# Optimization experiments

Measured on AMD Instinct MI355X. Metric: run time of the kernel, lower is better.

The kernel has to match this reference:

```python
import jax, jax.numpy as jnp
import numpy as np

TOP_K = 2
SCALING = 32.0 / 64.0  # lora_alpha / reservoir_size


def setup_inputs() -> dict:
    key = jax.random.key(0)
    ks = jax.random.split(key, 6)
    Bsz, S, Din, Dout, R, E = 4, 2048, 4096, 4096, 64, 16
    x = jax.random.normal(ks[0], (Bsz, S, Din), dtype=jnp.float32)
    base_w = jax.random.normal(ks[1], (Dout, Din), dtype=jnp.float32) * 0.02
    base_b = jax.random.normal(ks[2], (Dout,), dtype=jnp.float32) * 0.02
    A = jax.random.normal(ks[3], (R, Din), dtype=jnp.float32) * (1.0 / np.sqrt(Din))
    B = jax.random.normal(ks[4], (E, Dout, R), dtype=jnp.float32) * 0.02
    router_w = jax.random.normal(ks[5], (E, Din), dtype=jnp.float32) * 0.02
    return {"x": x, "base_w": base_w, "base_b": base_b, "A": A, "B": B, "router_w": router_w}


def reference(x, base_w, base_b, A, B, router_w):
    # base linear: [b,s,din] @ [dout,din]^T + bias
    base_out = jnp.einsum('bsi,oi->bso', x, base_w) + base_b
    # low-rank projection through fixed reservoir A (activation=identity, dropout off)
    res_hidden = jnp.einsum('bsi,ri->bsr', x, A)          # [b,s,r]
    # routing
    logits = jnp.einsum('bsi,ei->bse', x, router_w)       # [b,s,E]
    probs = jax.nn.softmax(logits, axis=-1)
    topw, topi = jax.lax.top_k(probs, TOP_K)              # [b,s,k]
    topw = topw / (jnp.sum(topw, axis=-1, keepdims=True) + 1e-6)
    num_experts = B.shape[0]
    # combine weights per expert: sum_k w_k * onehot(idx_k)  -> [b,s,E]
    combine = jnp.sum(jax.nn.one_hot(topi, num_experts, dtype=x.dtype) * topw[..., None], axis=-2)
    # weighted per-expert lowrank B matmul and combine
    delta = jnp.einsum('bse,bsr,eor->bso', combine, res_hidden, B)
    return base_out + delta * SCALING
```

## Files before the change

### kernel.cpp

```cpp
#include <hip/hip_runtime.h>
#include <cstdint>
#include <cstddef>

typedef short short8 __attribute__((ext_vector_type(8)));
typedef float f32x4 __attribute__((ext_vector_type(4)));
typedef float f32x16 __attribute__((ext_vector_type(16)));

#define DIN  4096
#define DOUT 4096
#define RANK 64
#define NEXP 16
#define NTOK 8192
#define KCAT 5120
#define NKT  (KCAT / 64)
#define ROWB (KCAT * 2)

__device__ __forceinline__ unsigned short f2bf(float f) {
    unsigned int u = __builtin_bit_cast(unsigned int, f);
    u = (u + 0x7FFFu + ((u >> 16) & 1u)) >> 16;
    return (unsigned short)u;
}
__device__ __forceinline__ void async_cp16(const void* g, void* lds) {
    __builtin_amdgcn_global_load_lds(
        (const __attribute__((address_space(1))) void*)g,
        (__attribute__((address_space(3))) void*)lds, 16, 0, 0);
}

__global__ void __launch_bounds__(256) prep_all_kernel(
        const float* __restrict__ x, const float* __restrict__ rw,
        const float* __restrict__ bw, const float* __restrict__ Bm,
        const float* __restrict__ Am,
        unsigned short* __restrict__ Xcat, unsigned short* __restrict__ Wcat,
        unsigned short* __restrict__ W1A, float* __restrict__ Lg) {
    __shared__ __align__(16) float xsl[8][532];
    __shared__ __align__(16) float red[8][16][16];
    const int tid = threadIdx.x;

    if (blockIdx.x < 1024) {
        const int t0 = blockIdx.x * 8;
        const int tt = tid >> 5, l32 = tid & 31;
        const int eg = tid >> 6, ts = (tid >> 4) & 3, cc = tid & 15;
        float part[2][4] = {};

        for (int w = 0; w < 8; ++w) {
            #pragma unroll
            for (int sub = 0; sub < 4; ++sub) {
                const int col = w * 512 + sub * 128 + l32 * 4;
                const float4 xv = *(const float4*)&x[(size_t)(t0 + tt) * DIN + col];
                unsigned short b0 = f2bf(xv.x), b1 = f2bf(xv.y),
                               b2 = f2bf(xv.z), b3 = f2bf(xv.w);
                uint2 pk = { (unsigned)b0 | ((unsigned)b1 << 16),
                             (unsigned)b2 | ((unsigned)b3 << 16) };
                *(uint2*)&Xcat[(size_t)(t0 + tt) * KCAT + col] = pk;
                *(float4*)&xsl[tt][sub * 128 + l32 * 4] = xv;
            }
            __syncthreads();
            #pragma unroll
            for (int j = 0; j < 8; ++j) {
                const int colb = w * 512 + (j * 16 + cc) * 4;
                const float4 r0 = *(const float4*)&rw[(size_t)(eg * 4 + 0) * DIN + colb];
                const float4 r1 = *(const float4*)&rw[(size_t)(eg * 4 + 1) * DIN + colb];
                const float4 r2 = *(const float4*)&rw[(size_t)(eg * 4 + 2) * DIN + colb];
                const float4 r3 = *(const float4*)&rw[(size_t)(eg * 4 + 3) * DIN + colb];
                #pragma unroll
                for (int t2 = 0; t2 < 2; ++t2) {
                    const int t = ts * 2 + t2;
                    const float4 xv = *(const float4*)&xsl[t][(j * 16 + cc) * 4];
                    part[t2][0] += xv.x * r0.x + xv.y * r0.y + xv.z * r0.z + xv.w * r0.w;
                    part[t2][1] += xv.x * r1.x + xv.y * r1.y + xv.z * r1.z + xv.w * r1.w;
                    part[t2][2] += xv.x * r2.x + xv.y * r2.y + xv.z * r2.z + xv.w * r2.w;
                    part[t2][3] += xv.x * r3.x + xv.y * r3.y + xv.z * r3.z + xv.w * r3.w;
                }
            }
            __syncthreads();
        }
        #pragma unroll
        for (int t2 = 0; t2 < 2; ++t2)
            #pragma unroll
            for (int e = 0; e < 4; ++e)
                red[ts * 2 + t2][eg * 4 + e][cc] = part[t2][e];
        __syncthreads();
        if (tid < 128) {
            const int t = tid >> 4, e = tid & 15;
            float s = 0.f;
            #pragma unroll
            for (int c = 0; c < 16; ++c) s += red[t][e][c];
            Lg[(size_t)(t0 + t) * NEXP + e] = s;
        }
    } else {
        const unsigned NG1 = (unsigned)DOUT * KCAT / 8u;
        const unsigned NGT = NG1 + 64u * DIN / 8u;
        for (unsigned g = (blockIdx.x - 1024) * 256u + tid; g < NGT;
             g += 2048u * 256u) {
            const float* src;
            unsigned short* dst;
            if (g < NG1) {
                unsigned o  = g / 640u;
                unsigned c8 = (g - o * 640u) * 8u;
                dst = Wcat + (size_t)o * KCAT + c8;
                if (c8 < DIN) {
                    src = bw + (size_t)o * DIN + c8;
                } else {
                    unsigned cc2 = c8 - DIN;
                    unsigned e = cc2 >> 6, r = cc2 & 63u;
                    src = Bm + ((size_t)e * DOUT + o) * RANK + r;
                }
            } else {
                unsigned g2 = g - NG1;
                unsigned row = g2 >> 9;
                unsigned c8  = (g2 & 511u) * 8u;
                dst = W1A + (size_t)row * DIN + c8;
                src = Am + (size_t)row * DIN + c8;
            }
            float4 v0 = *(const float4*)(src);
            float4 v1 = *(const float4*)(src + 4);
            uint4 pk;
            pk.x = (unsigned)f2bf(v0.x) | ((unsigned)f2bf(v0.y) << 16);
            pk.y = (unsigned)f2bf(v0.z) | ((unsigned)f2bf(v0.w) << 16);
            pk.z = (unsigned)f2bf(v1.x) | ((unsigned)f2bf(v1.y) << 16);
            pk.w = (unsigned)f2bf(v1.z) | ((unsigned)f2bf(v1.w) << 16);
            *(uint4*)dst = pk;
        }
    }
}

__global__ void __launch_bounds__(256) proj_moe_kernel(
        const unsigned short* __restrict__ Xcat,
        const unsigned short* __restrict__ W1A,
        const float* __restrict__ Lg, unsigned short* __restrict__ XcatW) {
    __shared__ __align__(16) unsigned short Xs[16 * 128];
    __shared__ __align__(16) unsigned short Ws[64 * 128];
    __shared__ __align__(16) float cw[16][16];
    __shared__ __align__(16) float hbuf[16][68];
    const int tid = threadIdx.x;
    const int wave = tid >> 6, lane = tid & 63;
    const int quad = lane >> 4, l16 = lane & 15;
    const int t0 = blockIdx.x * 16;

    const int rX = tid >> 4, cXs = tid & 15;
    const int cX = (cXs & 8) | ((cXs ^ rX) & 7);

    if (tid < 16) {
        float l[16];
        #pragma unroll
        for (int e = 0; e < 16; ++e) l[e] = Lg[(size_t)(t0 + tid) * NEXP + e];
        int i1 = 0; float b1v = l[0];
        #pragma unroll
        for (int e = 1; e < 16; ++e) if (l[e] > b1v) { b1v = l[e]; i1 = e; }
        int i2 = -1; float b2v = -1e30f;
        #pragma unroll
        for (int e = 0; e < 16; ++e) if (e != i1 && l[e] > b2v) { b2v = l[e]; i2 = e; }
        float S = 0.f;
        #pragma unroll
        for (int e = 0; e < 16; ++e) S += expf(l[e] - b1v);
        const float p1 = 1.0f / S;
        const float p2 = expf(b2v - b1v) / S;
        const float d = p1 + p2 + 1e-6f;
        const float c1 = 0.5f * p1 / d;
        const float c2 = 0.5f * p2 / d;
        #pragma unroll
        for (int e = 0; e < 16; ++e)
            cw[tid][e] = (e == i1) ? c1 : (e == i2) ? c2 : 0.0f;
    }

    f32x4 acc = {};
    for (int kt = 0; kt < DIN / 128; ++kt) {
        const int k0 = kt * 128;
        async_cp16(Xcat + (size_t)(t0 + rX) * KCAT + k0 + cX * 8,
                   (char*)Xs + wave * 1024);
        #pragma unroll
        for (int i = 0; i < 4; ++i) {
            const int s = i * 256 + tid;
            const int rW = s >> 4, cWs = s & 15;
            const int cWc = (cWs & 8) | ((cWs ^ rW) & 7);
            async_cp16(W1A + (size_t)rW * DIN + k0 + cWc * 8,
                       (char*)Ws + i * 4096 + wave * 1024);
        }
        __syncthreads();
        #pragma unroll
        for (int kk = 0; kk < 4; ++kk) {
            const int c = kk * 4 + quad;
            const int sa = ((c & 8) | ((c ^ l16) & 7)) << 3;
            const int rb = wave * 16 + l16;
            const int sb = ((c & 8) | ((c ^ rb) & 7)) << 3;
            short8 am = *(const short8*)&Xs[l16 * 128 + sa];
            short8 bn = *(const short8*)&Ws[rb * 128 + sb];
            acc = __builtin_amdgcn_mfma_f32_16x16x32_bf16(am, bn, acc, 0, 0, 0);
        }
        __syncthreads();
    }
    #pragma unroll
    for (int r = 0; r < 4; ++r)
        hbuf[quad * 4 + r][wave * 16 + l16] = acc[r];
    __syncthreads();
    const int t = tid >> 4, e = tid & 15;
    const float c = cw[t][e];
    unsigned short* dst = XcatW + (size_t)(t0 + t) * KCAT + DIN + e * 64;
    #pragma unroll
    for (int r8 = 0; r8 < 8; ++r8) {
        unsigned short o16[8];
        #pragma unroll
        for (int k = 0; k < 8; ++k)
            o16[k] = f2bf(c * hbuf[t][r8 * 8 + k]);
        uint4 pk;
        pk.x = (unsigned)o16[0] | ((unsigned)o16[1] << 16);
        pk.y = (unsigned)o16[2] | ((unsigned)o16[3] << 16);
        pk.z = (unsigned)o16[4] | ((unsigned)o16[5] << 16);
        pk.w = (unsigned)o16[6] | ((unsigned)o16[7] << 16);
        *(uint4*)(dst + r8 * 8) = pk;
    }
}

__global__ void __launch_bounds__(512, 2) gemm_main_kernel(
        const unsigned short* __restrict__ Xcat,
        const unsigned short* __restrict__ Wcat,
        const float* __restrict__ bias, float* __restrict__ out) {
    __shared__ __align__(16) unsigned short As[2][256 * 64];
    __shared__ __align__(16) unsigned short Bs[2][256 * 64];

    const int tid  = threadIdx.x;
    const int wave = tid >> 6, lane = tid & 63;
    const int r5   = lane & 31, hi = lane >> 5, xb = r5 & 7;
    const int wm   = wave >> 2, wn = wave & 3;

    const int bid = blockIdx.x;
    const int swz = (bid & 7) * 64 + (bid >> 3);
    const int bm0 = (swz & 31) * 256;
    const int bn0 = (swz >> 5) * 256;

    const int urr = tid >> 3;
    const int cks = (tid & 7) ^ (urr & 7);
    const unsigned voffG = (unsigned)(urr * KCAT + cks * 8) * 2u;

    const char* gA = (const char*)Xcat + (size_t)bm0 * ROWB + voffG;
    const char* gB = (const char*)Wcat + (size_t)bn0 * ROWB + voffG;
    char* const ldsA  = (char*)&As[0][0];
    char* const ldsB  = (char*)&Bs[0][0];
    char* const ldswA = ldsA + wave * 1024;
    char* const ldswB = ldsB + wave * 1024;

#define STAGE_A(H, TT, BOFF2) { \
    async_cp16(gA + (size_t)((H) * 64) * ROWB + (size_t)(TT) * 128, \
               ldswA + (BOFF2) + (H) * 8192); \
    async_cp16(gA + (size_t)((H) * 64 + 128) * ROWB + (size_t)(TT) * 128, \
               ldswA + (BOFF2) + (H) * 8192 + 16384); }
#define STAGE_B(U, TT, BOFF2) { \
    async_cp16(gB + (size_t)((U) * 128) * ROWB + (size_t)(TT) * 128, \
               ldswB + (BOFF2) + (U) * 16384); \
    async_cp16(gB + (size_t)((U) * 128 + 64) * ROWB + (size_t)(TT) * 128, \
               ldswB + (BOFF2) + (U) * 16384 + 8192); }

    int vA[4], vB[4];
    #pragma unroll
    for (int kk = 0; kk < 4; ++kk) {
        const int vb = r5 * 128 + (((2 * kk + hi) ^ xb) * 16);
        vA[kk] = vb + wm * 8192;
        vB[kk] = vb + wn * 8192;
    }

    f32x16 acc00 = {}, acc01 = {}, acc10 = {}, acc11 = {};
    f32x16 acc20 = {}, acc21 = {}, acc30 = {}, acc31 = {};
    short8 bf0[4], bf1[4], fE[4], fO[4];

#define PREF_AF(DST, Q, BOFF2) { \
    _Pragma("unroll") \
    for (int kk = 0; kk < 4; ++kk) \
        DST[kk] = *(const short8*)(ldsA + (BOFF2) + vA[kk] + \
                                   ((Q) >> 1) * 16384 + ((Q) & 1) * 4096); }
#define MFMA8(AF, A0, A1) { \
    __builtin_amdgcn_s_setprio(1); \
    _Pragma("unroll") \
    for (int kk = 0; kk < 4; ++kk) { \
        A0 = __builtin_amdgcn_mfma_f32_32x32x16_bf16(AF[kk], bf0[kk], A0, 0, 0, 0); \
        A1 = __builtin_amdgcn_mfma_f32_32x32x16_bf16(AF[kk], bf1[kk], A1, 0, 0, 0); \
    } \
    __builtin_amdgcn_s_setprio(0); }
#define CLOB asm volatile("" ::: "memory")
#define BAR  __builtin_amdgcn_s_barrier()
#define LGKM0 { asm volatile("s_waitcnt lgkmcnt(0)" ::: "memory"); \
                __builtin_amdgcn_sched_barrier(0); }
#define SBAR __builtin_amdgcn_sched_barrier(0)

    STAGE_B(0, 0, 0);     STAGE_B(1, 0, 0);
    STAGE_A(0, 0, 0);     STAGE_A(1, 0, 0);
    STAGE_B(0, 1, 32768); STAGE_B(1, 1, 32768);
    STAGE_A(0, 1, 32768);
    asm volatile("s_waitcnt vmcnt(6)" ::: "memory");
    CLOB; BAR; CLOB;

    #pragma unroll 2
    for (int t = 0; t < NKT; ++t) {
        const int boff = (t & 1) * 32768;
        const int ob   = boff ^ 32768;
        const int ts1  = (t + 1 < NKT) ? t + 1 : t;
        const int ts2  = (t + 2 < NKT) ? t + 2 : t;

        #pragma unroll
        for (int kk = 0; kk < 4; ++kk) {
            bf0[kk] = *(const short8*)(ldsB + boff + vB[kk]);
            bf1[kk] = *(const short8*)(ldsB + boff + vB[kk] + 4096);
            fE[kk]  = *(const short8*)(ldsA + boff + vA[kk]);
        }
        STAGE_A(1, ts1, ob);
        CLOB; BAR;
        LGKM0;
        PREF_AF(fO, 1, boff); SBAR;
        MFMA8(fE, acc00, acc01);
        SBAR; CLOB; BAR;

        STAGE_B(0, ts2, boff);
        CLOB; BAR;
        LGKM0;
        PREF_AF(fE, 2, boff); SBAR;
        MFMA8(fO, acc10, acc11);
        SBAR; CLOB; BAR;

        STAGE_B(1, ts2, boff);
        CLOB; BAR;
        LGKM0;
        PREF_AF(fO, 3, boff); SBAR;
        MFMA8(fE, acc20, acc21);
        SBAR; CLOB; BAR;

        STAGE_A(0, ts2, boff);
        CLOB; BAR;
        LGKM0;
        MFMA8(fO, acc30, acc31);
        SBAR;
        asm volatile("s_waitcnt vmcnt(6)" ::: "memory");
        CLOB; BAR;
    }

#define EPI(Q, A0, A1) { \
    const int rb = bm0 + ((Q) >> 1) * 128 + wm * 64 + ((Q) & 1) * 32 + 4 * hi; \
    { const int col = bn0 + wn * 64 + r5; const float bj = bias[col]; \
      _Pragma("unroll") for (int r = 0; r < 16; ++r) { \
        const int row = rb + (r & 3) + 8 * (r >> 2); \
        out[(size_t)row * DOUT + col] = A0[r] + bj; } } \
    { const int col = bn0 + wn * 64 + 32 + r5; const float bj = bias[col]; \
      _Pragma("unroll") for (int r = 0; r < 16; ++r) { \
        const int row = rb + (r & 3) + 8 * (r >> 2); \
        out[(size_t)row * DOUT + col] = A1[r] + bj; } } }
    EPI(0, acc00, acc01)
    EPI(1, acc10, acc11)
    EPI(2, acc20, acc21)
    EPI(3, acc30, acc31)
#undef STAGE_A
#undef STAGE_B
#undef PREF_AF
#undef MFMA8
#undef CLOB
#undef BAR
#undef LGKM0
#undef SBAR
#undef EPI
}

extern "C" void kernel_launch(void* const* d_in, const int* in_sizes, int n_in,
                              void* d_out, int out_size, void* d_ws, size_t ws_size,
                              hipStream_t stream) {
    const float* x  = (const float*)d_in[0];
    const float* bw = (const float*)d_in[1];
    const float* bb = (const float*)d_in[2];
    const float* Am = (const float*)d_in[3];
    const float* Bm = (const float*)d_in[4];
    const float* rw = (const float*)d_in[5];
    float* out = (float*)d_out;
    char* ws = (char*)d_ws;
    unsigned short* Xcat = (unsigned short*)(ws);
    unsigned short* Wcat = (unsigned short*)(ws + 83886080);
    unsigned short* W1A  = (unsigned short*)(ws + 125829120);
    float* Lg = (float*)(ws + 126353408);

    hipLaunchKernelGGL(prep_all_kernel, dim3(3072),   dim3(256), 0, stream,
                       x, rw, bw, Bm, Am, Xcat, Wcat, W1A, Lg);
    hipLaunchKernelGGL(proj_moe_kernel, dim3(512),    dim3(256), 0, stream,
                       Xcat, W1A, Lg, Xcat);
    hipLaunchKernelGGL(gemm_main_kernel, dim3(512),   dim3(512), 0, stream,
                       Xcat, Wcat, bb, out);
}
```

Before: 660.6 us.

## Switch main GEMM from 32x32x16 to 16x16x32 MFMA with new fragment layout

Rewrites the inner compute of the main bf16 GEMM to use 16x16x32 MFMA instructions instead of 32x32x16. The LDS fragment addressing, accumulator layout (8x4 f32x4 tiles per wave) and epilogue store mapping change to match. The first A fragment for the next k-tile is now prefetched at the end of each iteration, before the last MFMA group. The aim is higher MFMA throughput on this hardware and better overlap of LDS reads with compute. The trade-off is more MFMA instructions to issue, different LDS bank access patterns, and a different, less contiguous output write pattern.

```diff
diff --git a/kernel.cpp b/kernel.cpp
--- a/kernel.cpp
+++ b/kernel.cpp
@@ -4,7 +4,6 @@
 
 typedef short short8 __attribute__((ext_vector_type(8)));
 typedef float f32x4 __attribute__((ext_vector_type(4)));
-typedef float f32x16 __attribute__((ext_vector_type(16)));
 
 #define DIN  4096
 #define DOUT 4096
@@ -220,7 +219,7 @@
 
     const int tid  = threadIdx.x;
     const int wave = tid >> 6, lane = tid & 63;
-    const int r5   = lane & 31, hi = lane >> 5, xb = r5 & 7;
+    const int l16  = lane & 15, quad = lane >> 4, xb = l16 & 7;
     const int wm   = wave >> 2, wn = wave & 3;
 
     const int bid = blockIdx.x;
@@ -250,30 +249,37 @@
     async_cp16(gB + (size_t)((U) * 128 + 64) * ROWB + (size_t)(TT) * 128, \
                ldswB + (BOFF2) + (U) * 16384 + 8192); }
 
-    int vA[4], vB[4];
-    #pragma unroll
-    for (int kk = 0; kk < 4; ++kk) {
-        const int vb = r5 * 128 + (((2 * kk + hi) ^ xb) * 16);
-        vA[kk] = vb + wm * 8192;
-        vB[kk] = vb + wn * 8192;
-    }
-
-    f32x16 acc00 = {}, acc01 = {}, acc10 = {}, acc11 = {};
-    f32x16 acc20 = {}, acc21 = {}, acc30 = {}, acc31 = {};
-    short8 bf0[4], bf1[4], fE[4], fO[4];
-
-#define PREF_AF(DST, Q, BOFF2) { \
+    const int kof0 = ((quad)     ^ xb) * 16;
+    const int kof1 = ((4 + quad) ^ xb) * 16;
+    const char* ldsAw = ldsA + wm * 16384 + l16 * 128;
+    const char* ldsBw = ldsB + wn * 8192  + l16 * 128;
+
+    f32x4 acc[8][4] = {};
+    short8 bf[8];
+    short8 fE[4], fO[4];
+
+#define READ_BF(BOFF2) { \
     _Pragma("unroll") \
-    for (int kk = 0; kk < 4; ++kk) \
-        DST[kk] = *(const short8*)(ldsA + (BOFF2) + vA[kk] + \
-                                   ((Q) >> 1) * 16384 + ((Q) & 1) * 4096); }
-#define MFMA8(AF, A0, A1) { \
+    for (int n = 0; n < 4; ++n) { \
+        bf[n * 2 + 0] = *(const short8*)(ldsBw + (BOFF2) + n * 2048 + kof0); \
+        bf[n * 2 + 1] = *(const short8*)(ldsBw + (BOFF2) + n * 2048 + kof1); \
+    } }
+#define PREF_A(DST, Q, BOFF2) { \
+    _Pragma("unroll") \
+    for (int mm = 0; mm < 2; ++mm) { \
+        DST[mm * 2 + 0] = *(const short8*)(ldsAw + (BOFF2) + (2 * (Q) + mm) * 2048 + kof0); \
+        DST[mm * 2 + 1] = *(const short8*)(ldsAw + (BOFF2) + (2 * (Q) + mm) * 2048 + kof1); \
+    } }
+#define MFMA16(AF, Q) { \
     __builtin_amdgcn_s_setprio(1); \
     _Pragma("unroll") \
-    for (int kk = 0; kk < 4; ++kk) { \
-        A0 = __builtin_amdgcn_mfma_f32_32x32x16_bf16(AF[kk], bf0[kk], A0, 0, 0, 0); \
-        A1 = __builtin_amdgcn_mfma_f32_32x32x16_bf16(AF[kk], bf1[kk], A1, 0, 0, 0); \
-    } \
+    for (int kk = 0; kk < 2; ++kk) \
+        _Pragma("unroll") \
+        for (int mm = 0; mm < 2; ++mm) \
+            _Pragma("unroll") \
+            for (int n = 0; n < 4; ++n) \
+                acc[2 * (Q) + mm][n] = __builtin_amdgcn_mfma_f32_16x16x32_bf16( \
+                    AF[mm * 2 + kk], bf[n * 2 + kk], acc[2 * (Q) + mm][n], 0, 0, 0); \
     __builtin_amdgcn_s_setprio(0); }
 #define CLOB asm volatile("" ::: "memory")
 #define BAR  __builtin_amdgcn_s_barrier()
@@ -287,6 +293,7 @@
     STAGE_A(0, 1, 32768);
     asm volatile("s_waitcnt vmcnt(6)" ::: "memory");
     CLOB; BAR; CLOB;
+    PREF_A(fE, 0, 0);
 
     #pragma unroll 2
     for (int t = 0; t < NKT; ++t) {
@@ -295,65 +302,57 @@
         const int ts1  = (t + 1 < NKT) ? t + 1 : t;
         const int ts2  = (t + 2 < NKT) ? t + 2 : t;
 
-        #pragma unroll
-        for (int kk = 0; kk < 4; ++kk) {
-            bf0[kk] = *(const short8*)(ldsB + boff + vB[kk]);
-            bf1[kk] = *(const short8*)(ldsB + boff + vB[kk] + 4096);
-            fE[kk]  = *(const short8*)(ldsA + boff + vA[kk]);
-        }
+        READ_BF(boff);
         STAGE_A(1, ts1, ob);
         CLOB; BAR;
         LGKM0;
-        PREF_AF(fO, 1, boff); SBAR;
-        MFMA8(fE, acc00, acc01);
+        PREF_A(fO, 1, boff); SBAR;
+        MFMA16(fE, 0);
         SBAR; CLOB; BAR;
 
         STAGE_B(0, ts2, boff);
         CLOB; BAR;
         LGKM0;
-        PREF_AF(fE, 2, boff); SBAR;
-        MFMA8(fO, acc10, acc11);
+        PREF_A(fE, 2, boff); SBAR;
+        MFMA16(fO, 1);
         SBAR; CLOB; BAR;
 
         STAGE_B(1, ts2, boff);
         CLOB; BAR;
         LGKM0;
-        PREF_AF(fO, 3, boff); SBAR;
-        MFMA8(fE, acc20, acc21);
+        PREF_A(fO, 3, boff); SBAR;
+        MFMA16(fE, 2);
         SBAR; CLOB; BAR;
 
         STAGE_A(0, ts2, boff);
         CLOB; BAR;
         LGKM0;
-        MFMA8(fO, acc30, acc31);
-        SBAR;
         asm volatile("s_waitcnt vmcnt(6)" ::: "memory");
-        CLOB; BAR;
-    }
-
-#define EPI(Q, A0, A1) { \
-    const int rb = bm0 + ((Q) >> 1) * 128 + wm * 64 + ((Q) & 1) * 32 + 4 * hi; \
-    { const int col = bn0 + wn * 64 + r5; const float bj = bias[col]; \
-      _Pragma("unroll") for (int r = 0; r < 16; ++r) { \
-        const int row = rb + (r & 3) + 8 * (r >> 2); \
-        out[(size_t)row * DOUT + col] = A0[r] + bj; } } \
-    { const int col = bn0 + wn * 64 + 32 + r5; const float bj = bias[col]; \
-      _Pragma("unroll") for (int r = 0; r < 16; ++r) { \
-        const int row = rb + (r & 3) + 8 * (r >> 2); \
-        out[(size_t)row * DOUT + col] = A1[r] + bj; } } }
-    EPI(0, acc00, acc01)
-    EPI(1, acc10, acc11)
-    EPI(2, acc20, acc21)
-    EPI(3, acc30, acc31)
+        PREF_A(fE, 0, ob); SBAR;
+        MFMA16(fO, 3);
+        SBAR; CLOB; BAR;
+    }
+
+    const int orow = bm0 + wm * 128 + quad * 4;
+    #pragma unroll
+    for (int n = 0; n < 4; ++n) {
+        const int col = bn0 + wn * 64 + n * 16 + l16;
+        const float bj = bias[col];
+        #pragma unroll
+        for (int m = 0; m < 8; ++m)
+            #pragma unroll
+            for (int r = 0; r < 4; ++r)
+                out[(size_t)(orow + m * 16 + r) * DOUT + col] = acc[m][n][r] + bj;
+    }
 #undef STAGE_A
 #undef STAGE_B
-#undef PREF_AF
-#undef MFMA8
+#undef READ_BF
+#undef PREF_A
+#undef MFMA16
 #undef CLOB
 #undef BAR
 #undef LGKM0
 #undef SBAR
-#undef EPI
 }
 
 extern "C" void kernel_launch(void* const* d_in, const int* in_sizes, int n_in,
```

After: 667.5 us. Within noise of the previous version (+1.0%).
